# Kernel tuning notes

Hardware: AMD Instinct MI355X
Metric: run time of the kernel (lower is better)

The kernel has to match this reference:

```python
import jax, jax.numpy as jnp
import numpy as np

C_SPARSITY = 3.0  # repo default
N_BLOCKS_1 = 128   # layer_inputs // granularity
IN_PER_BLK_1 = 64  # granularity
LAYER_OUTPUTS = 8192

def setup_inputs() -> dict:
    key = jax.random.key(0)
    k_x, k_c1, k_c2 = jax.random.split(key, 3)
    x = jax.random.normal(k_x, (4096, 8192), dtype=jnp.float32)
    # c_sub_layer_1: [n_blocks_1, inputs_per_block_1, outputs_per_block_1]
    c1 = jax.random.normal(k_c1, (128, 64, 64), dtype=jnp.float32)
    # c_sub_layer_2: [n_blocks_2, inputs_per_block_2, outputs_per_block_2]
    c2 = jax.random.normal(k_c2, (64, 128, 128), dtype=jnp.float32)
    return {"x": x, "c1": c1, "c2": c2}

def reference(x, c1, c2):
    # Softmax-gated connectivity over the input axis of each block (dim=1)
    conn_1 = jax.nn.softmax(c1 * C_SPARSITY, axis=1)  # [n, i, m]
    conn_2 = jax.nn.softmax(c2 * C_SPARSITY, axis=1)  # [m, n, o]
    b = x.shape[0]
    x_r = x.reshape(b, N_BLOCKS_1, IN_PER_BLK_1)  # [b, n, i]
    # Two-stage block-diagonal interconnect (Monarch-like)
    t = jnp.einsum('bni,nim->bnm', x_r, conn_1)   # [b, n, m]
    out = jnp.einsum('bnm,mno->bmo', t, conn_2)   # [b, m, o]
    return out.reshape(b, LAYER_OUTPUTS)
```

## Files before the change

### kernel.cpp

```cpp
#include <hip/hip_runtime.h>

#define BATCH     4096
#define N1        128
#define I1        64
#define MMID      64
#define OOUT      128
#define LDX       8192
#define CSP       3.0f

typedef _Float16 half8  __attribute__((ext_vector_type(8)));
typedef float    float4_ __attribute__((ext_vector_type(4)));
typedef unsigned int uint4_ __attribute__((ext_vector_type(4)));

__global__ __launch_bounds__(256) void prep_kernel(
    const float* __restrict__ c1, const float* __restrict__ c2,
    _Float16* __restrict__ conn1T, _Float16* __restrict__ conn2T) {
  int gid = blockIdx.x * 256 + threadIdx.x;
  if (gid < N1 * MMID) {
    const float* p = c1 + (size_t)(gid >> 6) * (I1 * MMID) + (gid & 63);
    float mx = -1e30f;
    for (int i = 0; i < I1; ++i) mx = fmaxf(mx, p[i * MMID]);
    mx *= CSP;
    float s = 0.f;
    for (int i = 0; i < I1; ++i) s += __expf(p[i * MMID] * CSP - mx);
    float inv = 1.0f / s;
    _Float16* dst = conn1T + (size_t)gid * I1;
    for (int i = 0; i < I1; ++i)
      dst[i] = (_Float16)(__expf(p[i * MMID] * CSP - mx) * inv);
  } else {
    int g = gid - N1 * MMID;
    if (g < MMID * OOUT) {
      const float* p = c2 + (size_t)(g >> 7) * (N1 * OOUT) + (g & 127);
      float mx = -1e30f;
      for (int i = 0; i < N1; ++i) mx = fmaxf(mx, p[i * OOUT]);
      mx *= CSP;
      float s = 0.f;
      for (int i = 0; i < N1; ++i) s += __expf(p[i * OOUT] * CSP - mx);
      float inv = 1.0f / s;
      _Float16* dst = conn2T + (size_t)g * N1;
      for (int i = 0; i < N1; ++i)
        dst[i] = (_Float16)(__expf(p[i * OOUT] * CSP - mx) * inv);
    }
  }
}

#define S1_MSTRIDE 34
#define S1_BSTRIDE (64 * S1_MSTRIDE + 4)

__global__ __launch_bounds__(256) void stage1_kernel(
    const float* __restrict__ x, const _Float16* __restrict__ conn1T,
    _Float16* __restrict__ t2) {
  __shared__ _Float16 lbuf[16 * S1_BSTRIDE];

  const int b0   = blockIdx.x * 16;
  const int n0   = blockIdx.y * 32;
  const int tid  = threadIdx.x;
  const int lane = tid & 63;
  const int wave = tid >> 6;
  const int row  = lane & 15;
  const int quad = lane >> 4;
  const int kk   = quad * 8;
  const int m_col = wave * 16 + row;

  const float* xrow = x + (size_t)(b0 + row) * LDX;

  for (int nn = 0; nn < 32; ++nn) {
    const int n = n0 + nn;
    const float* ap = xrow + n * I1 + kk;
    float4_ a0lo = *(const float4_*)(ap);
    float4_ a0hi = *(const float4_*)(ap + 4);
    float4_ a1lo = *(const float4_*)(ap + 32);
    float4_ a1hi = *(const float4_*)(ap + 36);
    half8 a0, a1;
#pragma unroll
    for (int j = 0; j < 4; ++j) {
      a0[j]     = (_Float16)a0lo[j];
      a0[j + 4] = (_Float16)a0hi[j];
      a1[j]     = (_Float16)a1lo[j];
      a1[j + 4] = (_Float16)a1hi[j];
    }
    const _Float16* bp = conn1T + ((size_t)n * MMID + m_col) * I1 + kk;
    half8 bf0 = *(const half8*)(bp);
    half8 bf1 = *(const half8*)(bp + 32);

    float4_ acc = {0.f, 0.f, 0.f, 0.f};
    acc = __builtin_amdgcn_mfma_f32_16x16x32_f16(a0, bf0, acc, 0, 0, 0);
    acc = __builtin_amdgcn_mfma_f32_16x16x32_f16(a1, bf1, acc, 0, 0, 0);

#pragma unroll
    for (int r = 0; r < 4; ++r) {
      int bl = quad * 4 + r;
      lbuf[bl * S1_BSTRIDE + m_col * S1_MSTRIDE + nn] = (_Float16)acc[r];
    }
  }
  __syncthreads();

#pragma unroll
  for (int it = 0; it < 4; ++it) {
    int p  = tid + it * 256;
    int bl = p >> 6;
    int mm = p & 63;
    const unsigned int* src =
        (const unsigned int*)(lbuf + bl * S1_BSTRIDE + mm * S1_MSTRIDE);
    uint4_ v0 = {src[0],  src[1],  src[2],  src[3]};
    uint4_ v1 = {src[4],  src[5],  src[6],  src[7]};
    uint4_ v2 = {src[8],  src[9],  src[10], src[11]};
    uint4_ v3 = {src[12], src[13], src[14], src[15]};
    _Float16* dst = t2 + ((size_t)(b0 + bl) * MMID + mm) * N1 + n0;
    *(uint4_*)(dst)      = v0;
    *(uint4_*)(dst + 8)  = v1;
    *(uint4_*)(dst + 16) = v2;
    *(uint4_*)(dst + 24) = v3;
  }
}

__global__ __launch_bounds__(256) void stage2_kernel(
    const _Float16* __restrict__ t2, const _Float16* __restrict__ conn2T,
    float* __restrict__ out) {
  const int m    = blockIdx.x;
  const int b0   = blockIdx.y * 64;
  const int tid  = threadIdx.x;
  const int lane = tid & 63;
  const int wave = tid >> 6;
  const int row  = lane & 15;
  const int quad = lane >> 4;

  const int b = b0 + wave * 16 + row;
  const _Float16* arow  = t2 + ((size_t)b * MMID + m) * N1;
  const _Float16* bbase = conn2T + (size_t)m * OOUT * N1;

  float4_ acc[8];
#pragma unroll
  for (int ot = 0; ot < 8; ++ot) acc[ot] = (float4_){0.f, 0.f, 0.f, 0.f};

#pragma unroll
  for (int ks = 0; ks < 4; ++ks) {
    const int kk = ks * 32 + quad * 8;
    half8 a = *(const half8*)(arow + kk);
#pragma unroll
    for (int ot = 0; ot < 8; ++ot) {
      const int o = ot * 16 + row;
      half8 bf = *(const half8*)(bbase + (size_t)o * N1 + kk);
      acc[ot] = __builtin_amdgcn_mfma_f32_16x16x32_f16(a, bf, acc[ot], 0, 0, 0);
    }
  }

#pragma unroll
  for (int ot = 0; ot < 8; ++ot) {
#pragma unroll
    for (int r = 0; r < 4; ++r) {
      const int bb = b0 + wave * 16 + quad * 4 + r;
      const int o  = ot * 16 + row;
      out[(size_t)bb * LDX + m * OOUT + o] = acc[ot][r];
    }
  }
}

extern "C" void kernel_launch(void* const* d_in, const int* in_sizes, int n_in,
                              void* d_out, int out_size, void* d_ws, size_t ws_size,
                              hipStream_t stream) {
  (void)in_sizes; (void)n_in; (void)out_size; (void)ws_size;
  const float* x  = (const float*)d_in[0];
  const float* c1 = (const float*)d_in[1];
  const float* c2 = (const float*)d_in[2];
  float* out = (float*)d_out;

  _Float16* conn1T = (_Float16*)d_ws;
  _Float16* conn2T = conn1T + (size_t)N1 * MMID * I1;
  _Float16* t2     = conn2T + (size_t)MMID * OOUT * N1;

  prep_kernel<<<64, 256, 0, stream>>>(c1, c2, conn1T, conn2T);
  stage1_kernel<<<dim3(BATCH / 16, N1 / 32), 256, 0, stream>>>(x, conn1T, t2);
  stage2_kernel<<<dim3(MMID, BATCH / 64), 256, 0, stream>>>(t2, conn2T, out);
}
```

Before: 400.3 us.

## Restructure stage1 to split n-blocks across waves and chunk t2 layout

Stage1 now gives each wave 4 of the block's 16 n-blocks, computing all 64 m-columns per wave. Before, every wave looped over all 32 n-blocks and redundantly reloaded and converted the same x data. The intermediate t2 is stored as contiguous 16-wide chunks per n-group, and stage2 reads it in that layout. Stage2 also hoists all A and B fragment loads ahead of the MFMA chain to expose memory-level parallelism, at the cost of more registers. The grid doubles along n, and each block loads x only once, cutting redundant x traffic.

```diff
diff --git a/kernel.cpp b/kernel.cpp
--- a/kernel.cpp
+++ b/kernel.cpp
@@ -44,7 +44,8 @@
   }
 }
 
-#define S1_MSTRIDE 34
+#define S1_NC      16
+#define S1_MSTRIDE 18
 #define S1_BSTRIDE (64 * S1_MSTRIDE + 4)
 
 __global__ __launch_bounds__(256) void stage1_kernel(
@@ -53,19 +54,21 @@
   __shared__ _Float16 lbuf[16 * S1_BSTRIDE];
 
   const int b0   = blockIdx.x * 16;
-  const int n0   = blockIdx.y * 32;
+  const int c    = blockIdx.y;
+  const int n0   = c * S1_NC;
   const int tid  = threadIdx.x;
   const int lane = tid & 63;
   const int wave = tid >> 6;
   const int row  = lane & 15;
   const int quad = lane >> 4;
   const int kk   = quad * 8;
-  const int m_col = wave * 16 + row;
 
   const float* xrow = x + (size_t)(b0 + row) * LDX;
 
-  for (int nn = 0; nn < 32; ++nn) {
-    const int n = n0 + nn;
+#pragma unroll 2
+  for (int j = 0; j < 4; ++j) {
+    const int nn = wave * 4 + j;
+    const int n  = n0 + nn;
     const float* ap = xrow + n * I1 + kk;
     float4_ a0lo = *(const float4_*)(ap);
     float4_ a0hi = *(const float4_*)(ap + 4);
@@ -73,24 +76,30 @@
     float4_ a1hi = *(const float4_*)(ap + 36);
     half8 a0, a1;
 #pragma unroll
-    for (int j = 0; j < 4; ++j) {
-      a0[j]     = (_Float16)a0lo[j];
-      a0[j + 4] = (_Float16)a0hi[j];
-      a1[j]     = (_Float16)a1lo[j];
-      a1[j + 4] = (_Float16)a1hi[j];
+    for (int u = 0; u < 4; ++u) {
+      a0[u]     = (_Float16)a0lo[u];
+      a0[u + 4] = (_Float16)a0hi[u];
+      a1[u]     = (_Float16)a1lo[u];
+      a1[u + 4] = (_Float16)a1hi[u];
     }
-    const _Float16* bp = conn1T + ((size_t)n * MMID + m_col) * I1 + kk;
-    half8 bf0 = *(const half8*)(bp);
-    half8 bf1 = *(const half8*)(bp + 32);
-
-    float4_ acc = {0.f, 0.f, 0.f, 0.f};
-    acc = __builtin_amdgcn_mfma_f32_16x16x32_f16(a0, bf0, acc, 0, 0, 0);
-    acc = __builtin_amdgcn_mfma_f32_16x16x32_f16(a1, bf1, acc, 0, 0, 0);
-
+    const _Float16* bn = conn1T + (size_t)n * (MMID * I1);
+    half8 bf0[4], bf1[4];
 #pragma unroll
-    for (int r = 0; r < 4; ++r) {
-      int bl = quad * 4 + r;
-      lbuf[bl * S1_BSTRIDE + m_col * S1_MSTRIDE + nn] = (_Float16)acc[r];
+    for (int mt = 0; mt < 4; ++mt) {
+      const _Float16* bp = bn + (mt * 16 + row) * I1 + kk;
+      bf0[mt] = *(const half8*)(bp);
+      bf1[mt] = *(const half8*)(bp + 32);
+    }
+#pragma unroll
+    for (int mt = 0; mt < 4; ++mt) {
+      float4_ acc = {0.f, 0.f, 0.f, 0.f};
+      acc = __builtin_amdgcn_mfma_f32_16x16x32_f16(a0, bf0[mt], acc, 0, 0, 0);
+      acc = __builtin_amdgcn_mfma_f32_16x16x32_f16(a1, bf1[mt], acc, 0, 0, 0);
+#pragma unroll
+      for (int r = 0; r < 4; ++r) {
+        lbuf[(quad * 4 + r) * S1_BSTRIDE + (mt * 16 + row) * S1_MSTRIDE + nn] =
+            (_Float16)acc[r];
+      }
     }
   }
   __syncthreads();
@@ -102,15 +111,12 @@
     int mm = p & 63;
     const unsigned int* src =
         (const unsigned int*)(lbuf + bl * S1_BSTRIDE + mm * S1_MSTRIDE);
-    uint4_ v0 = {src[0],  src[1],  src[2],  src[3]};
-    uint4_ v1 = {src[4],  src[5],  src[6],  src[7]};
-    uint4_ v2 = {src[8],  src[9],  src[10], src[11]};
-    uint4_ v3 = {src[12], src[13], src[14], src[15]};
-    _Float16* dst = t2 + ((size_t)(b0 + bl) * MMID + mm) * N1 + n0;
-    *(uint4_*)(dst)      = v0;
-    *(uint4_*)(dst + 8)  = v1;
-    *(uint4_*)(dst + 16) = v2;
-    *(uint4_*)(dst + 24) = v3;
+    uint4_ v0 = {src[0], src[1], src[2], src[3]};
+    uint4_ v1 = {src[4], src[5], src[6], src[7]};
+    _Float16* dst =
+        t2 + (((size_t)c * BATCH + b0 + bl) * MMID + mm) * S1_NC;
+    *(uint4_*)(dst)     = v0;
+    *(uint4_*)(dst + 8) = v1;
   }
 }
 
@@ -126,24 +132,31 @@
   const int quad = lane >> 4;
 
   const int b = b0 + wave * 16 + row;
-  const _Float16* arow  = t2 + ((size_t)b * MMID + m) * N1;
+  half8 a[4];
+#pragma unroll
+  for (int ks = 0; ks < 4; ++ks) {
+    const int cc  = ks * 2 + (quad >> 1);
+    const int off = (quad & 1) * 8;
+    a[ks] = *(const half8*)(
+        t2 + (((size_t)cc * BATCH + b) * MMID + m) * S1_NC + off);
+  }
   const _Float16* bbase = conn2T + (size_t)m * OOUT * N1;
+  half8 bf[4][8];
+#pragma unroll
+  for (int ks = 0; ks < 4; ++ks)
+#pragma unroll
+    for (int ot = 0; ot < 8; ++ot)
+      bf[ks][ot] =
+          *(const half8*)(bbase + (size_t)(ot * 16 + row) * N1 + ks * 32 + quad * 8);
 
   float4_ acc[8];
 #pragma unroll
   for (int ot = 0; ot < 8; ++ot) acc[ot] = (float4_){0.f, 0.f, 0.f, 0.f};
-
 #pragma unroll
-  for (int ks = 0; ks < 4; ++ks) {
-    const int kk = ks * 32 + quad * 8;
-    half8 a = *(const half8*)(arow + kk);
+  for (int ks = 0; ks < 4; ++ks)
 #pragma unroll
-    for (int ot = 0; ot < 8; ++ot) {
-      const int o = ot * 16 + row;
-      half8 bf = *(const half8*)(bbase + (size_t)o * N1 + kk);
-      acc[ot] = __builtin_amdgcn_mfma_f32_16x16x32_f16(a, bf, acc[ot], 0, 0, 0);
-    }
-  }
+    for (int ot = 0; ot < 8; ++ot)
+      acc[ot] = __builtin_amdgcn_mfma_f32_16x16x32_f16(a[ks], bf[ks][ot], acc[ot], 0, 0, 0);
 
 #pragma unroll
   for (int ot = 0; ot < 8; ++ot) {
@@ -170,6 +183,6 @@
   _Float16* t2     = conn2T + (size_t)MMID * OOUT * N1;
 
   prep_kernel<<<64, 256, 0, stream>>>(c1, c2, conn1T, conn2T);
-  stage1_kernel<<<dim3(BATCH / 16, N1 / 32), 256, 0, stream>>>(x, conn1T, t2);
+  stage1_kernel<<<dim3(BATCH / 16, N1 / S1_NC), 256, 0, stream>>>(x, conn1T, t2);
   stage2_kernel<<<dim3(MMID, BATCH / 64), 256, 0, stream>>>(t2, conn2T, out);
 }
```

Result: faster. 359.3 us (-10.2%).
